# Kernel tuning notes

Hardware: AMD Instinct MI355X
Metric: run time of the kernel (lower is better)

Reference implementation:

```python
import jax, jax.numpy as jnp
import numpy as np

W = 10       # workspace_size
ORDER = 2    # quantum-neuron order
STAGES = 2
N_QUBITS = W + ORDER
N_IN = 6     # number of input lanes (len(input))
BATCH = 512


def ry_mat(theta):
    # real rY(theta) = [[cos(t/2), -sin(t/2)], [sin(t/2), cos(t/2)]]
    c = jnp.cos(theta / 2)
    s = jnp.sin(theta / 2)
    return jnp.stack([jnp.stack([c, -s]), jnp.stack([s, c])])


def apply_1q(psi, G, lane):
    # apply 2x2 gate G to qubit `lane` of psi with shape (B, 2, ..., 2)
    ax = lane + 1
    out = jnp.tensordot(G, psi, axes=((1,), (ax,)))  # contracted axis becomes axis 0
    return jnp.moveaxis(out, 0, ax)


def apply_cry(psi, theta, control, target):
    # controlled-rY(theta): rotate target only in the control==1 half of the state
    axc = control + 1
    psi0, psi1 = jnp.split(psi, 2, axis=axc)  # size-1 control axis kept -> lane indices unchanged
    psi1 = apply_1q(psi1, ry_mat(theta), target)
    return jnp.concatenate([psi0, psi1], axis=axc)


def neuron_apply(psi, theta, outlane):
    # Quantum neuron (Cao et al. / Bausch RQNN), measurement-free recursion of depth ORDER.
    # theta: (W+1,) = W input weights + 1 bias. Ancillas live on lanes W .. W+ORDER-1.
    def rot_block(p, sign):
        for i in range(W):
            p = apply_cry(p, sign * theta[i], i, W)  # crY from workspace lane i onto ancilla 0
        return apply_1q(p, ry_mat(sign * theta[W]), W)  # bias rotation on ancilla 0

    def recurse(p, d, sign):
        if d == 0:
            return rot_block(p, sign)
        t = outlane if d == ORDER else W + d
        p = recurse(p, d - 1, 1.0)
        p = apply_cry(p, sign * np.pi, W + d - 1, t)  # controlled-(iY) = crY(pi); inverse = crY(-pi)
        return recurse(p, d - 1, -1.0)

    return recurse(psi, ORDER, 1.0)


def setup_inputs() -> dict:
    key = jax.random.key(0)
    k1, k2, k3, k4 = jax.random.split(key, 4)
    psi = jax.random.normal(k1, (BATCH,) + (2,) * N_QUBITS, dtype=jnp.float32)
    norm = jnp.sqrt((psi ** 2).sum(axis=tuple(range(1, psi.ndim)), keepdims=True))
    psi = psi / norm  # normalized real quantum state per batch element
    inp = jax.random.randint(k2, (N_IN,), 0, 2)
    unitary_theta = jax.random.normal(k3, (STAGES, W), dtype=jnp.float32)
    neuron_theta = jax.random.normal(k4, (STAGES, W, W + 1), dtype=jnp.float32)
    return {"psi": psi, "inp": inp, "unitary_theta": unitary_theta, "neuron_theta": neuron_theta}


def reference(psi, inp, unitary_theta, neuron_theta):
    # BitFlipLayer: X (axis reversal) on input lanes whose bit is 1
    for l in range(N_IN):
        psi = jnp.where(inp[l] == 1, jnp.flip(psi, axis=l + 1), psi)
    # stages of (UnitaryLayer, then one QuantumNeuronLayer per workspace lane)
    for s in range(STAGES):
        for i in range(W):
            psi = apply_1q(psi, ry_mat(unitary_theta[s, i]), i)
        for out in range(W):
            psi = neuron_apply(psi, neuron_theta[s, out], out)
    # probabilities over the input lanes: marginal |amplitude|^2
    probs = (psi ** 2).sum(axis=tuple(range(N_IN + 1, psi.ndim)))  # (B, 2,...,2) over input lanes
    probs = probs.reshape(psi.shape[0], -1)  # (B, 2**N_IN)
    return probs, psi
```

## Files before the change

### kernel.cpp

```cpp
#include <hip/hip_runtime.h>
#include <math.h>


typedef float v2f __attribute__((ext_vector_type(2)));

#define NSLOT 512

__device__ __forceinline__ v2f mk(float a, float b) { v2f r; r.x = a; r.y = b; return r; }

__device__ __forceinline__ void fast_sincos(float a, float* s, float* c) {
    float r = a * 0.15915494309189535f;
    *s = __builtin_amdgcn_sinf(r);
    *c = __builtin_amdgcn_cosf(r);
}

template <int XM>
__device__ __forceinline__ float shx(float x) {
    if constexpr (XM == 1) {
        return __int_as_float(__builtin_amdgcn_update_dpp(
            0, __float_as_int(x), 0xB1, 0xF, 0xF, true));
    } else if constexpr (XM == 2) {
        return __int_as_float(__builtin_amdgcn_update_dpp(
            0, __float_as_int(x), 0x4E, 0xF, 0xF, true));
    } else if constexpr (XM == 8) {
        return __int_as_float(__builtin_amdgcn_update_dpp(
            0, __float_as_int(x), 0x128, 0xF, 0xF, true));
    } else {
        return __shfl_xor(x, XM, 64);
    }
}

template <int LM>
__device__ __forceinline__ void lane_ry_t(v2f (&V)[4], float c, float s, int ln) {
    float ss = (ln & LM) ? s : -s;
#pragma unroll
    for (int k = 0; k < 4; ++k) {
        v2f p = mk(shx<LM>(V[k].x), shx<LM>(V[k].y));
        V[k] = c * V[k] + ss * p;
    }
}

__device__ __forceinline__ void wave_ry(v2f (&V)[4], int wm, float c, float s,
                                        int wv, int ln, float4* buf) {
    const int slot = wv * 64 + ln;
    buf[slot]         = make_float4(V[0].x, V[0].y, V[1].x, V[1].y);
    buf[NSLOT + slot] = make_float4(V[2].x, V[2].y, V[3].x, V[3].y);
    __syncthreads();
    const int pslot = (wv ^ wm) * 64 + ln;
    float ss = (wv & wm) ? s : -s;
    float4 t0 = buf[pslot];
    float4 t1 = buf[NSLOT + pslot];
    V[0] = c * V[0] + ss * mk(t0.x, t0.y);
    V[1] = c * V[1] + ss * mk(t0.z, t0.w);
    V[2] = c * V[2] + ss * mk(t1.x, t1.y);
    V[3] = c * V[3] + ss * mk(t1.z, t1.w);
}

__device__ __forceinline__ void half1(v2f V0, v2f V1, float c, float s,
                                      v2f& u0, v2f& u1) {
    v2f t0 = c * V0 - s * V1;
    v2f t1 = s * V0 + c * V1;
    v2f t1s = __builtin_shufflevector(t1, t1, 1, 0);
    u0 =  c * t0 + mk(-s,  s) * t1s;
    u1 = -s * t0 + mk(-c,  c) * t1s;
}

__device__ __forceinline__ void half2(v2f& V0, v2f& V1, float c, float s,
                                      v2f u0, v2f u1) {
    v2f r0 = c * u0 - s * u1;
    v2f r1 = s * u0 + c * u1;
    v2f r1s = __builtin_shufflevector(r1, r1, 1, 0);
    V0 =  c * r0 + mk( s, -s) * r1s;
    V1 = -s * r0 + mk( c, -c) * r1s;
}

template <int OUT>
__device__ __forceinline__ void neuron(v2f (&V)[4], const float* __restrict__ th,
                                       int wv, int ln, float4* buf) {
    float a0 = (ln & 32) ? th[0] : 0.f;
    float a1 = (ln & 16) ? th[1] : 0.f;
    float a2 = (ln &  8) ? th[2] : 0.f;
    float a3 = (ln &  4) ? th[3] : 0.f;
    float a4 = (ln &  2) ? th[4] : 0.f;
    float a5 = (ln &  1) ? th[5] : 0.f;
    float wsum = th[10];
    if (wv & 4) wsum += th[6];
    if (wv & 2) wsum += th[7];
    if (wv & 1) wsum += th[8];
    float phih = 0.5f * (((a0 + a1) + (a2 + a3)) + ((a4 + a5) + wsum));

    float sA, cA, sB, cB;
    fast_sincos(phih, &sA, &cA);
    fast_sincos(phih + 0.5f * th[9], &sB, &cB);

    v2f uA0, uA1, uB0, uB1;
    half1(V[0], V[1], cA, sA, uA0, uA1);
    half1(V[2], V[3], cB, sB, uB0, uB1);

    if constexpr (OUT < 6) {
        constexpr int LM = 1 << (5 - OUT);
        float ss = (ln & LM) ? 1.f : -1.f;
        uA0.y = ss * shx<LM>(uA0.y);
        uA1.y = ss * shx<LM>(uA1.y);
        uB0.y = ss * shx<LM>(uB0.y);
        uB1.y = ss * shx<LM>(uB1.y);
    } else if constexpr (OUT < 9) {
        constexpr int WM = 1 << (8 - OUT);
        const int slot = wv * 64 + ln;
        buf[slot] = make_float4(uA0.y, uA1.y, uB0.y, uB1.y);
        __syncthreads();
        const int pslot = (wv ^ WM) * 64 + ln;
        float ss = (wv & WM) ? 1.f : -1.f;
        float4 t = buf[pslot];
        uA0.y = ss * t.x; uA1.y = ss * t.y; uB0.y = ss * t.z; uB1.y = ss * t.w;
    } else {
        float t1 = uA0.y, t3 = uA1.y;
        uA0.y = -uB0.y; uA1.y = -uB1.y;
        uB0.y = t1;     uB1.y = t3;
    }

    half2(V[0], V[1], cA, sA, uA0, uA1);
    half2(V[2], V[3], cB, sB, uB0, uB1);
}

__global__ __launch_bounds__(512, 4) void rvqe_kernel(
    const float* __restrict__ psi_in,
    const int*   __restrict__ inp,
    const float* __restrict__ ut,
    const float* __restrict__ nt,
    float* __restrict__ out_probs,
    float* __restrict__ out_psi)
{
    __shared__ float4 xbuf[2][2 * NSLOT];

    const int b   = blockIdx.x;
    const int tid = threadIdx.x;
    const int ln  = tid & 63;
    const int wv  = tid >> 6;
    int bi = 0;

    int flip = 0;
#pragma unroll
    for (int l = 0; l < 6; ++l)
        if (inp[l] == 1) flip |= 1 << (5 - l);

    v2f V[4];
    {
        const float* src = psi_in + (size_t)b * 4096 + (((ln ^ flip) & 63) << 6) + (wv << 3);
        float4 t0 = ((const float4*)src)[0];
        float4 t1 = ((const float4*)src)[1];
        V[0] = mk(t0.x, t0.y); V[1] = mk(t0.z, t0.w);
        V[2] = mk(t1.x, t1.y); V[3] = mk(t1.z, t1.w);
    }

    for (int s = 0; s < 2; ++s) {
        const float* uts = ut + s * 10;
        const float* nts = nt + (size_t)s * 110;

        {
            float cc, ss;
            fast_sincos(0.5f * uts[0], &ss, &cc); lane_ry_t<32>(V, cc, ss, ln);
            fast_sincos(0.5f * uts[1], &ss, &cc); lane_ry_t<16>(V, cc, ss, ln);
            fast_sincos(0.5f * uts[2], &ss, &cc); lane_ry_t<8>(V, cc, ss, ln);
            fast_sincos(0.5f * uts[3], &ss, &cc); lane_ry_t<4>(V, cc, ss, ln);
            fast_sincos(0.5f * uts[4], &ss, &cc); lane_ry_t<2>(V, cc, ss, ln);
            fast_sincos(0.5f * uts[5], &ss, &cc); lane_ry_t<1>(V, cc, ss, ln);
            fast_sincos(0.5f * uts[6], &ss, &cc);
            wave_ry(V, 4, cc, ss, wv, ln, xbuf[bi]); bi ^= 1;
            fast_sincos(0.5f * uts[7], &ss, &cc);
            wave_ry(V, 2, cc, ss, wv, ln, xbuf[bi]); bi ^= 1;
            fast_sincos(0.5f * uts[8], &ss, &cc);
            wave_ry(V, 1, cc, ss, wv, ln, xbuf[bi]); bi ^= 1;
            fast_sincos(0.5f * uts[9], &ss, &cc);
            v2f n0 = cc * V[0] - ss * V[2];
            v2f n2 = ss * V[0] + cc * V[2];
            v2f n1 = cc * V[1] - ss * V[3];
            v2f n3 = ss * V[1] + cc * V[3];
            V[0] = n0; V[1] = n1; V[2] = n2; V[3] = n3;
        }

        neuron<0>(V, nts + 0 * 11, wv, ln, nullptr);
        neuron<1>(V, nts + 1 * 11, wv, ln, nullptr);
        neuron<2>(V, nts + 2 * 11, wv, ln, nullptr);
        neuron<3>(V, nts + 3 * 11, wv, ln, nullptr);
        neuron<4>(V, nts + 4 * 11, wv, ln, nullptr);
        neuron<5>(V, nts + 5 * 11, wv, ln, nullptr);
        neuron<6>(V, nts + 6 * 11, wv, ln, xbuf[bi]); bi ^= 1;
        neuron<7>(V, nts + 7 * 11, wv, ln, xbuf[bi]); bi ^= 1;
        neuron<8>(V, nts + 8 * 11, wv, ln, xbuf[bi]); bi ^= 1;
        neuron<9>(V, nts + 9 * 11, wv, ln, nullptr);
    }

    float acc = 0.f;
#pragma unroll
    for (int k = 0; k < 4; ++k) acc += V[k].x * V[k].x + V[k].y * V[k].y;
    {
        float* pb = (float*)&xbuf[bi][0];
        pb[wv * 64 + ln] = acc;
        __syncthreads();
        if (wv == 0) {
            float t = 0.f;
#pragma unroll
            for (int w = 0; w < 8; ++w) t += pb[w * 64 + ln];
            out_probs[(size_t)b * 64 + ln] = t;
        }
    }

    float* dst = out_psi + (size_t)b * 4096 + (ln << 6) + (wv << 3);
    ((float4*)dst)[0] = make_float4(V[0].x, V[0].y, V[1].x, V[1].y);
    ((float4*)dst)[1] = make_float4(V[2].x, V[2].y, V[3].x, V[3].y);
}

extern "C" void kernel_launch(void* const* d_in, const int* in_sizes, int n_in,
                              void* d_out, int out_size, void* d_ws, size_t ws_size,
                              hipStream_t stream) {
    const float* psi = (const float*)d_in[0];
    const int*   inp = (const int*)d_in[1];
    const float* ut  = (const float*)d_in[2];
    const float* nt  = (const float*)d_in[3];

    const int B = in_sizes[0] >> 12;
    float* probs = (float*)d_out;
    float* opsi  = probs + (size_t)B * 64;

    rvqe_kernel<<<B, 512, 0, stream>>>(psi, inp, ut, nt, probs, opsi);
}
```

Measured before the change: 84.49 us.

## Split state across 16 waves per block with four amplitudes per thread

```diff
diff --git a/kernel.cpp b/kernel.cpp
--- a/kernel.cpp
+++ b/kernel.cpp
@@ -4,7 +4,7 @@
 
 typedef float v2f __attribute__((ext_vector_type(2)));
 
-#define NSLOT 512
+#define NSLOT 1024
 
 __device__ __forceinline__ v2f mk(float a, float b) { v2f r; r.x = a; r.y = b; return r; }
 
@@ -31,29 +31,23 @@
 }
 
 template <int LM>
-__device__ __forceinline__ void lane_ry_t(v2f (&V)[4], float c, float s, int ln) {
+__device__ __forceinline__ void lane_ry_t(v2f& V0, v2f& V1, float c, float s, int ln) {
     float ss = (ln & LM) ? s : -s;
-#pragma unroll
-    for (int k = 0; k < 4; ++k) {
-        v2f p = mk(shx<LM>(V[k].x), shx<LM>(V[k].y));
-        V[k] = c * V[k] + ss * p;
-    }
-}
-
-__device__ __forceinline__ void wave_ry(v2f (&V)[4], int wm, float c, float s,
+    v2f p0 = mk(shx<LM>(V0.x), shx<LM>(V0.y));
+    v2f p1 = mk(shx<LM>(V1.x), shx<LM>(V1.y));
+    V0 = c * V0 + ss * p0;
+    V1 = c * V1 + ss * p1;
+}
+
+__device__ __forceinline__ void wave_ry(v2f& V0, v2f& V1, int wm, float c, float s,
                                         int wv, int ln, float4* buf) {
     const int slot = wv * 64 + ln;
-    buf[slot]         = make_float4(V[0].x, V[0].y, V[1].x, V[1].y);
-    buf[NSLOT + slot] = make_float4(V[2].x, V[2].y, V[3].x, V[3].y);
+    buf[slot] = make_float4(V0.x, V0.y, V1.x, V1.y);
     __syncthreads();
-    const int pslot = (wv ^ wm) * 64 + ln;
+    float4 t = buf[(wv ^ wm) * 64 + ln];
     float ss = (wv & wm) ? s : -s;
-    float4 t0 = buf[pslot];
-    float4 t1 = buf[NSLOT + pslot];
-    V[0] = c * V[0] + ss * mk(t0.x, t0.y);
-    V[1] = c * V[1] + ss * mk(t0.z, t0.w);
-    V[2] = c * V[2] + ss * mk(t1.x, t1.y);
-    V[3] = c * V[3] + ss * mk(t1.z, t1.w);
+    V0 = c * V0 + ss * mk(t.x, t.y);
+    V1 = c * V1 + ss * mk(t.z, t.w);
 }
 
 __device__ __forceinline__ void half1(v2f V0, v2f V1, float c, float s,
@@ -75,8 +69,8 @@
 }
 
 template <int OUT>
-__device__ __forceinline__ void neuron(v2f (&V)[4], const float* __restrict__ th,
-                                       int wv, int ln, float4* buf) {
+__device__ __forceinline__ void neuron(v2f& V0, v2f& V1, const float* __restrict__ th,
+                                       int wv, int ln, float2* buf) {
     float a0 = (ln & 32) ? th[0] : 0.f;
     float a1 = (ln & 16) ? th[1] : 0.f;
     float a2 = (ln &  8) ? th[2] : 0.f;
@@ -84,46 +78,38 @@
     float a4 = (ln &  2) ? th[4] : 0.f;
     float a5 = (ln &  1) ? th[5] : 0.f;
     float wsum = th[10];
-    if (wv & 4) wsum += th[6];
-    if (wv & 2) wsum += th[7];
-    if (wv & 1) wsum += th[8];
+    if (wv & 8) wsum += th[6];
+    if (wv & 4) wsum += th[7];
+    if (wv & 2) wsum += th[8];
+    if (wv & 1) wsum += th[9];
     float phih = 0.5f * (((a0 + a1) + (a2 + a3)) + ((a4 + a5) + wsum));
 
-    float sA, cA, sB, cB;
-    fast_sincos(phih, &sA, &cA);
-    fast_sincos(phih + 0.5f * th[9], &sB, &cB);
-
-    v2f uA0, uA1, uB0, uB1;
-    half1(V[0], V[1], cA, sA, uA0, uA1);
-    half1(V[2], V[3], cB, sB, uB0, uB1);
+    float s, c;
+    fast_sincos(phih, &s, &c);
+
+    v2f u0, u1;
+    half1(V0, V1, c, s, u0, u1);
 
     if constexpr (OUT < 6) {
         constexpr int LM = 1 << (5 - OUT);
         float ss = (ln & LM) ? 1.f : -1.f;
-        uA0.y = ss * shx<LM>(uA0.y);
-        uA1.y = ss * shx<LM>(uA1.y);
-        uB0.y = ss * shx<LM>(uB0.y);
-        uB1.y = ss * shx<LM>(uB1.y);
-    } else if constexpr (OUT < 9) {
-        constexpr int WM = 1 << (8 - OUT);
+        u0.y = ss * shx<LM>(u0.y);
+        u1.y = ss * shx<LM>(u1.y);
+    } else {
+        constexpr int WM = 1 << (9 - OUT);
         const int slot = wv * 64 + ln;
-        buf[slot] = make_float4(uA0.y, uA1.y, uB0.y, uB1.y);
+        buf[slot] = make_float2(u0.y, u1.y);
         __syncthreads();
-        const int pslot = (wv ^ WM) * 64 + ln;
+        float2 t = buf[(wv ^ WM) * 64 + ln];
         float ss = (wv & WM) ? 1.f : -1.f;
-        float4 t = buf[pslot];
-        uA0.y = ss * t.x; uA1.y = ss * t.y; uB0.y = ss * t.z; uB1.y = ss * t.w;
-    } else {
-        float t1 = uA0.y, t3 = uA1.y;
-        uA0.y = -uB0.y; uA1.y = -uB1.y;
-        uB0.y = t1;     uB1.y = t3;
-    }
-
-    half2(V[0], V[1], cA, sA, uA0, uA1);
-    half2(V[2], V[3], cB, sB, uB0, uB1);
-}
-
-__global__ __launch_bounds__(512, 4) void rvqe_kernel(
+        u0.y = ss * t.x;
+        u1.y = ss * t.y;
+    }
+
+    half2(V0, V1, c, s, u0, u1);
+}
+
+__global__ __launch_bounds__(1024, 8) void rvqe_kernel(
     const float* __restrict__ psi_in,
     const int*   __restrict__ inp,
     const float* __restrict__ ut,
@@ -131,7 +117,7 @@
     float* __restrict__ out_probs,
     float* __restrict__ out_psi)
 {
-    __shared__ float4 xbuf[2][2 * NSLOT];
+    __shared__ float4 xbuf[2][NSLOT];
 
     const int b   = blockIdx.x;
     const int tid = threadIdx.x;
@@ -144,13 +130,11 @@
     for (int l = 0; l < 6; ++l)
         if (inp[l] == 1) flip |= 1 << (5 - l);
 
-    v2f V[4];
+    v2f V0, V1;
     {
-        const float* src = psi_in + (size_t)b * 4096 + (((ln ^ flip) & 63) << 6) + (wv << 3);
-        float4 t0 = ((const float4*)src)[0];
-        float4 t1 = ((const float4*)src)[1];
-        V[0] = mk(t0.x, t0.y); V[1] = mk(t0.z, t0.w);
-        V[2] = mk(t1.x, t1.y); V[3] = mk(t1.z, t1.w);
+        const float* src = psi_in + (size_t)b * 4096 + (((ln ^ flip) & 63) << 6) + (wv << 2);
+        float4 t = *(const float4*)src;
+        V0 = mk(t.x, t.y); V1 = mk(t.z, t.w);
     }
 
     for (int s = 0; s < 2; ++s) {
@@ -159,41 +143,35 @@
 
         {
             float cc, ss;
-            fast_sincos(0.5f * uts[0], &ss, &cc); lane_ry_t<32>(V, cc, ss, ln);
-            fast_sincos(0.5f * uts[1], &ss, &cc); lane_ry_t<16>(V, cc, ss, ln);
-            fast_sincos(0.5f * uts[2], &ss, &cc); lane_ry_t<8>(V, cc, ss, ln);
-            fast_sincos(0.5f * uts[3], &ss, &cc); lane_ry_t<4>(V, cc, ss, ln);
-            fast_sincos(0.5f * uts[4], &ss, &cc); lane_ry_t<2>(V, cc, ss, ln);
-            fast_sincos(0.5f * uts[5], &ss, &cc); lane_ry_t<1>(V, cc, ss, ln);
+            fast_sincos(0.5f * uts[0], &ss, &cc); lane_ry_t<32>(V0, V1, cc, ss, ln);
+            fast_sincos(0.5f * uts[1], &ss, &cc); lane_ry_t<16>(V0, V1, cc, ss, ln);
+            fast_sincos(0.5f * uts[2], &ss, &cc); lane_ry_t<8>(V0, V1, cc, ss, ln);
+            fast_sincos(0.5f * uts[3], &ss, &cc); lane_ry_t<4>(V0, V1, cc, ss, ln);
+            fast_sincos(0.5f * uts[4], &ss, &cc); lane_ry_t<2>(V0, V1, cc, ss, ln);
+            fast_sincos(0.5f * uts[5], &ss, &cc); lane_ry_t<1>(V0, V1, cc, ss, ln);
             fast_sincos(0.5f * uts[6], &ss, &cc);
-            wave_ry(V, 4, cc, ss, wv, ln, xbuf[bi]); bi ^= 1;
+            wave_ry(V0, V1, 8, cc, ss, wv, ln, xbuf[bi]); bi ^= 1;
             fast_sincos(0.5f * uts[7], &ss, &cc);
-            wave_ry(V, 2, cc, ss, wv, ln, xbuf[bi]); bi ^= 1;
+            wave_ry(V0, V1, 4, cc, ss, wv, ln, xbuf[bi]); bi ^= 1;
             fast_sincos(0.5f * uts[8], &ss, &cc);
-            wave_ry(V, 1, cc, ss, wv, ln, xbuf[bi]); bi ^= 1;
+            wave_ry(V0, V1, 2, cc, ss, wv, ln, xbuf[bi]); bi ^= 1;
             fast_sincos(0.5f * uts[9], &ss, &cc);
-            v2f n0 = cc * V[0] - ss * V[2];
-            v2f n2 = ss * V[0] + cc * V[2];
-            v2f n1 = cc * V[1] - ss * V[3];
-            v2f n3 = ss * V[1] + cc * V[3];
-            V[0] = n0; V[1] = n1; V[2] = n2; V[3] = n3;
+            wave_ry(V0, V1, 1, cc, ss, wv, ln, xbuf[bi]); bi ^= 1;
         }
 
-        neuron<0>(V, nts + 0 * 11, wv, ln, nullptr);
-        neuron<1>(V, nts + 1 * 11, wv, ln, nullptr);
-        neuron<2>(V, nts + 2 * 11, wv, ln, nullptr);
-        neuron<3>(V, nts + 3 * 11, wv, ln, nullptr);
-        neuron<4>(V, nts + 4 * 11, wv, ln, nullptr);
-        neuron<5>(V, nts + 5 * 11, wv, ln, nullptr);
-        neuron<6>(V, nts + 6 * 11, wv, ln, xbuf[bi]); bi ^= 1;
-        neuron<7>(V, nts + 7 * 11, wv, ln, xbuf[bi]); bi ^= 1;
-        neuron<8>(V, nts + 8 * 11, wv, ln, xbuf[bi]); bi ^= 1;
-        neuron<9>(V, nts + 9 * 11, wv, ln, nullptr);
-    }
-
-    float acc = 0.f;
-#pragma unroll
-    for (int k = 0; k < 4; ++k) acc += V[k].x * V[k].x + V[k].y * V[k].y;
+        neuron<0>(V0, V1, nts + 0 * 11, wv, ln, nullptr);
+        neuron<1>(V0, V1, nts + 1 * 11, wv, ln, nullptr);
+        neuron<2>(V0, V1, nts + 2 * 11, wv, ln, nullptr);
+        neuron<3>(V0, V1, nts + 3 * 11, wv, ln, nullptr);
+        neuron<4>(V0, V1, nts + 4 * 11, wv, ln, nullptr);
+        neuron<5>(V0, V1, nts + 5 * 11, wv, ln, nullptr);
+        neuron<6>(V0, V1, nts + 6 * 11, wv, ln, (float2*)xbuf[bi]); bi ^= 1;
+        neuron<7>(V0, V1, nts + 7 * 11, wv, ln, (float2*)xbuf[bi]); bi ^= 1;
+        neuron<8>(V0, V1, nts + 8 * 11, wv, ln, (float2*)xbuf[bi]); bi ^= 1;
+        neuron<9>(V0, V1, nts + 9 * 11, wv, ln, (float2*)xbuf[bi]); bi ^= 1;
+    }
+
+    float acc = V0.x * V0.x + V0.y * V0.y + V1.x * V1.x + V1.y * V1.y;
     {
         float* pb = (float*)&xbuf[bi][0];
         pb[wv * 64 + ln] = acc;
@@ -201,14 +179,13 @@
         if (wv == 0) {
             float t = 0.f;
 #pragma unroll
-            for (int w = 0; w < 8; ++w) t += pb[w * 64 + ln];
+            for (int w = 0; w < 16; ++w) t += pb[w * 64 + ln];
             out_probs[(size_t)b * 64 + ln] = t;
         }
     }
 
-    float* dst = out_psi + (size_t)b * 4096 + (ln << 6) + (wv << 3);
-    ((float4*)dst)[0] = make_float4(V[0].x, V[0].y, V[1].x, V[1].y);
-    ((float4*)dst)[1] = make_float4(V[2].x, V[2].y, V[3].x, V[3].y);
+    float* dst = out_psi + (size_t)b * 4096 + (ln << 6) + (wv << 2);
+    *(float4*)dst = make_float4(V0.x, V0.y, V1.x, V1.y);
 }
 
 extern "C" void kernel_launch(void* const* d_in, const int* in_sizes, int n_in,
@@ -223,5 +200,5 @@
     float* probs = (float*)d_out;
     float* opsi  = probs + (size_t)B * 64;
 
-    rvqe_kernel<<<B, 512, 0, stream>>>(psi, inp, ut, nt, probs, opsi);
-}
+    rvqe_kernel<<<B, 1024, 0, stream>>>(psi, inp, ut, nt, probs, opsi);
+}
```

Result: slower. 86.45 us (+2.3%).
